# Performance work log

Hardware: AMD Instinct MI355X
Metric: run time of the kernel (lower is better)

Reference implementation:

```python
import jax, jax.numpy as jnp
import numpy as np

D, H_DIM, HEADS = 512, 2048, 8

def rmsnorm(x, w):
    eps = jnp.finfo(x.dtype).eps
    return x * jax.lax.rsqrt(jnp.mean(x * x, axis=-1, keepdims=True) + eps) * w

def setup_inputs() -> dict:
    key = jax.random.key(0)
    ks = jax.random.split(key, 16)
    B, N = 2, 2048
    s_d = 1.0 / np.sqrt(D)
    s_h = 1.0 / np.sqrt(H_DIM)
    inp = {
        "x": jax.random.normal(ks[0], (B, N, D), jnp.float32),
        "DA": jax.random.randint(ks[1], (B, 1, N, N), 0, 2, jnp.int32),
        "Wq": jax.random.normal(ks[2], (D, D), jnp.float32) * s_d,
        "bq": jnp.zeros((D,), jnp.float32),
        "Wk": jax.random.normal(ks[3], (D, D), jnp.float32) * s_d,
        "bk": jnp.zeros((D,), jnp.float32),
        "Wv": jax.random.normal(ks[4], (D, D), jnp.float32) * s_d,
        "bv": jnp.zeros((D,), jnp.float32),
        "W1": jax.random.normal(ks[5], (H_DIM, D), jnp.float32) * s_d,
        "b1": jnp.zeros((H_DIM,), jnp.float32),
        "W2": jax.random.normal(ks[6], (H_DIM, D), jnp.float32) * s_d,
        "b2": jnp.zeros((H_DIM,), jnp.float32),
        "W3": jax.random.normal(ks[7], (D, H_DIM), jnp.float32) * s_h,
        "b3": jnp.zeros((D,), jnp.float32),
        "g1": jnp.ones((D,), jnp.float32),
        "g2": jnp.ones((D,), jnp.float32),
    }
    return inp

def reference(x, DA, Wq, bq, Wk, bk, Wv, bv, W1, b1, W2, b2, W3, b3, g1, g2):
    B, N, _ = x.shape
    hd = D // HEADS  # head_dim = 64
    xn = rmsnorm(x, g1)
    # projections (torch Linear: y = x @ W.T + b), split heads -> [B,H,N,hd]
    def split(t):
        return t.reshape(B, N, HEADS, hd).transpose(0, 2, 1, 3)
    q = split(xn @ Wq.T + bq)
    k = split(xn @ Wk.T + bk)
    v = split(xn @ Wv.T + bv)
    scores = jnp.einsum("bhnd,bhmd->bhnm", q, k) / np.sqrt(hd)
    scores = jnp.where(DA == 0, jnp.asarray(-1e20, scores.dtype), scores)
    attn = jax.nn.softmax(scores, axis=-1)
    o = jnp.einsum("bhnm,bhmd->bhnd", attn, v)
    o = o.transpose(0, 2, 1, 3).reshape(B, N, D)
    h = x + o
    hn = rmsnorm(h, g2)
    x2 = hn @ W1.T + b1
    x3 = hn @ W2.T + b2
    out = h + (jax.nn.silu(x2) * x3) @ W3.T + b3
    return out
```

## Files before the change

kernel.cpp:

```cpp
#include <hip/hip_runtime.h>

typedef unsigned short u16;
typedef unsigned int   u32;
typedef unsigned long long u64;

using bf16x8 = __attribute__((ext_vector_type(8))) __bf16;
using f32x4  = __attribute__((ext_vector_type(4))) float;
using us8    = __attribute__((ext_vector_type(8))) u16;
using us4v   = __attribute__((ext_vector_type(4))) u16;

#define NB_TOK   4096
#define DD       512
#define HDIM     2048
#define SEQ      2048
#define EPS_F32  1.1920929e-7f
#define SM_SHIFT 16.0f

__device__ __forceinline__ u16 f32_to_bf16(float f) {
  u32 u = __float_as_uint(f);
  u += 0x7fffu + ((u >> 16) & 1u);
  return (u16)(u >> 16);
}
__device__ __forceinline__ float bf16_to_f32(u16 h) {
  return __uint_as_float(((u32)h) << 16);
}
__device__ __forceinline__ bf16x8 ld_frag(const u16* p) {
  return __builtin_bit_cast(bf16x8, *(const us8*)p);
}
__device__ __forceinline__ void gload_lds16(const void* g, void* l) {
  __builtin_amdgcn_global_load_lds(
      (__attribute__((address_space(1))) void*)(void*)g,
      (__attribute__((address_space(3))) void*)l, 16, 0, 0);
}

__global__ __launch_bounds__(256) void k_pre(
    const float* __restrict__ wq, const float* __restrict__ wk,
    const float* __restrict__ wv, const float* __restrict__ w1,
    const float* __restrict__ w2, const float* __restrict__ w3,
    const int* __restrict__ da, const float* __restrict__ x,
    const float* __restrict__ g1,
    u16* __restrict__ wqkv, u16* __restrict__ w1b,
    u16* __restrict__ w2b, u16* __restrict__ w3b,
    u64* __restrict__ maskT, u16* __restrict__ xn) {
  int bx = blockIdx.x;
  if (bx < 3840) {
    int e = (bx * 256 + threadIdx.x) * 4;
    const float* src; u16* dst; int off;
    if      (e <  262144) { src = wq; dst = wqkv;          off = e; }
    else if (e <  524288) { src = wk; dst = wqkv + 262144; off = e -  262144; }
    else if (e <  786432) { src = wv; dst = wqkv + 524288; off = e -  524288; }
    else if (e < 1835008) { src = w1; dst = w1b;           off = e -  786432; }
    else if (e < 2883584) { src = w2; dst = w2b;           off = e - 1835008; }
    else                  { src = w3; dst = w3b;           off = e - 2883584; }
    float4 v = *(const float4*)(src + off);
    us4v o;
    o[0] = f32_to_bf16(v.x); o[1] = f32_to_bf16(v.y);
    o[2] = f32_to_bf16(v.z); o[3] = f32_to_bf16(v.w);
    *(us4v*)(dst + off) = o;
  } else if (bx < 4864) {
    int lane = threadIdx.x & 63, wave = threadIdx.x >> 6;
    int row = (bx - 3840) * 4 + wave;
    int b = row >> 11, r = row & 2047;
    const int* src = da + (size_t)row * SEQ;
    #pragma unroll 4
    for (int w = 0; w < 32; ++w) {
      int d = src[w * 64 + lane];
      u64 bal = __ballot(d != 0);
      if (lane == 0) maskT[((size_t)(b * 32 + w)) * SEQ + r] = bal;
    }
  } else {
    int lane = threadIdx.x & 63, wave = threadIdx.x >> 6;
    int row = (bx - 4864) * 4 + wave;
    size_t base = (size_t)row * DD + lane * 8;
    float4 a = *(const float4*)(x + base);
    float4 b = *(const float4*)(x + base + 4);
    float ss = a.x*a.x + a.y*a.y + a.z*a.z + a.w*a.w
             + b.x*b.x + b.y*b.y + b.z*b.z + b.w*b.w;
    #pragma unroll
    for (int m = 1; m < 64; m <<= 1) ss += __shfl_xor(ss, m);
    float sc = rsqrtf(ss * (1.0f / DD) + EPS_F32);
    float4 ga = *(const float4*)(g1 + lane * 8);
    float4 gb = *(const float4*)(g1 + lane * 8 + 4);
    us8 o;
    o[0] = f32_to_bf16(a.x * sc * ga.x); o[1] = f32_to_bf16(a.y * sc * ga.y);
    o[2] = f32_to_bf16(a.z * sc * ga.z); o[3] = f32_to_bf16(a.w * sc * ga.w);
    o[4] = f32_to_bf16(b.x * sc * gb.x); o[5] = f32_to_bf16(b.y * sc * gb.y);
    o[6] = f32_to_bf16(b.z * sc * gb.z); o[7] = f32_to_bf16(b.w * sc * gb.w);
    *(us8*)(xn + base) = o;
  }
}

template <int NB>
__device__ __forceinline__ void gemm_tile(const u16* __restrict__ A,
                                          const u16* const* Bm, int K,
                                          int mblk, int nblk, int kbeg, int kend,
                                          u16* lA, u16* lB,
                                          f32x4 (*acc)[4][4]) {
  const int tid = threadIdx.x, lane = tid & 63, wave = tid >> 6;
  const int l15 = lane & 15, quad = lane >> 4;
  const int wm = (wave >> 1) * 64, wn = (wave & 1) * 64;
  for (int k0 = kbeg; k0 < kend; k0 += 32) {
    #pragma unroll
    for (int i = 0; i < 2; ++i) {
      int s = wave * 2 + i;
      int row = s * 16 + l15;
      gload_lds16(A + (size_t)(mblk + row) * K + k0 + quad * 8, lA + s * 512);
      #pragma unroll
      for (int bi = 0; bi < NB; ++bi)
        gload_lds16(Bm[bi] + (size_t)(nblk + row) * K + k0 + quad * 8,
                    lB + bi * 4096 + s * 512);
    }
    __syncthreads();
    bf16x8 af[4], bf[NB][4];
    #pragma unroll
    for (int mt = 0; mt < 4; ++mt)
      af[mt] = ld_frag(lA + ((wm >> 4) + mt) * 512 + lane * 8);
    #pragma unroll
    for (int bi = 0; bi < NB; ++bi)
      #pragma unroll
      for (int nt = 0; nt < 4; ++nt)
        bf[bi][nt] = ld_frag(lB + bi * 4096 + ((wn >> 4) + nt) * 512 + lane * 8);
    #pragma unroll
    for (int bi = 0; bi < NB; ++bi)
      #pragma unroll
      for (int mt = 0; mt < 4; ++mt)
        #pragma unroll
        for (int nt = 0; nt < 4; ++nt)
          acc[bi][mt][nt] = __builtin_amdgcn_mfma_f32_16x16x32_bf16(
              af[mt], bf[bi][nt], acc[bi][mt][nt], 0, 0, 0);
    __syncthreads();
  }
}

__global__ __launch_bounds__(256) void k_qkv(const u16* __restrict__ xn,
                                             const u16* __restrict__ wqkv,
                                             const float* __restrict__ bq,
                                             const float* __restrict__ bk,
                                             const float* __restrict__ bv,
                                             u16* __restrict__ qb,
                                             u16* __restrict__ kb,
                                             u16* __restrict__ vt) {
  __shared__ u16 lA[4096], lB[4096];
  int z = blockIdx.z;
  const u16* Bp = wqkv + z * (DD * DD);
  const float* bias = (z == 0) ? bq : ((z == 1) ? bk : bv);
  float scale = (z == 0) ? 0.125f : 1.0f;
  int mblk = blockIdx.y * 128, nblk = blockIdx.x * 128;
  f32x4 acc[1][4][4];
  #pragma unroll
  for (int mt = 0; mt < 4; ++mt)
    #pragma unroll
    for (int nt = 0; nt < 4; ++nt) acc[0][mt][nt] = (f32x4)0.0f;
  const u16* Bs[1] = {Bp};
  gemm_tile<1>(xn, Bs, DD, mblk, nblk, 0, DD, lA, lB, acc);
  int lane = threadIdx.x & 63, wave = threadIdx.x >> 6;
  int l15 = lane & 15, quad = lane >> 4;
  int wm = (wave >> 1) * 64, wn = (wave & 1) * 64;
  if (z < 2) {
    u16* out = z ? kb : qb;
    #pragma unroll
    for (int mt = 0; mt < 4; ++mt)
      #pragma unroll
      for (int nt = 0; nt < 4; ++nt) {
        int n = nblk + wn + nt * 16 + l15;
        float bn = bias[n];
        #pragma unroll
        for (int r = 0; r < 4; ++r) {
          int m = mblk + wm + mt * 16 + quad * 4 + r;
          out[(size_t)m * DD + n] = f32_to_bf16((acc[0][mt][nt][r] + bn) * scale);
        }
      }
  } else {
    #pragma unroll
    for (int mt = 0; mt < 4; ++mt)
      #pragma unroll
      for (int nt = 0; nt < 4; ++nt) {
        int n = nblk + wn + nt * 16 + l15;
        float bn = bias[n];
        int m = mblk + wm + mt * 16 + quad * 4;
        int b = m >> 11, tok = m & 2047;
        us4v o;
        #pragma unroll
        for (int r = 0; r < 4; ++r) o[r] = f32_to_bf16(acc[0][mt][nt][r] + bn);
        *(us4v*)(vt + ((size_t)(b * 8 + (n >> 6)) * 64 + (n & 63)) * SEQ + tok) = o;
      }
  }
}

__global__ __launch_bounds__(256) void k_attn(const u16* __restrict__ q,
                                              const u16* __restrict__ k,
                                              const u16* __restrict__ vT,
                                              const u64* __restrict__ maskT,
                                              float* __restrict__ Opart,
                                              float* __restrict__ lpart) {
  __shared__ u16 lQ[4096], lK[8192], lV[8192], lP[4 * 16 * 72];
  int tid = threadIdx.x, lane = tid & 63, wave = tid >> 6;
  int l15 = lane & 15, quad = lane >> 4;
  int bh = blockIdx.y, b = bh >> 3, h = bh & 7;
  int q0 = blockIdx.x * 64;
  int z = blockIdx.z;
  int kvbase = z * 1024;
  const u16* qg = q + (size_t)(b * SEQ + q0) * DD + h * 64;
  const u16* kg = k + (size_t)(b * SEQ + kvbase) * DD + h * 64;
  const u16* vg = vT + (size_t)bh * 64 * SEQ + kvbase;
  const u64* mg = maskT + ((size_t)(b * 32 + z * 16)) * SEQ + q0 + wave * 16 + l15;

  #pragma unroll
  for (int i = 0; i < 2; ++i) {
    int s = wave * 2 + i;
    int row = (s >> 1) * 16 + l15, c = (s & 1) * 4 + quad;
    gload_lds16(qg + (size_t)row * DD + c * 8, lQ + s * 512);
    gload_lds16(kg + (size_t)row * DD + c * 8, lK + s * 512);
    gload_lds16(vg + (size_t)row * SEQ + c * 8, lV + s * 512);
  }
  __syncthreads();
  bf16x8 qa[2];
  qa[0] = ld_frag(lQ + wave * 1024 + lane * 8);
  qa[1] = ld_frag(lQ + wave * 1024 + 512 + lane * 8);

  f32x4 oa[4];
  #pragma unroll
  for (int r = 0; r < 4; ++r) oa[r] = (f32x4)0.0f;
  float ls = 0.0f;

  u16* pw = lP + wave * 1152;

  for (int t = 0; t < 16; ++t) {
    const u16* lKc = lK + (t & 1) * 4096;
    const u16* lVc = lV + (t & 1) * 4096;

    u64 mw = mg[(size_t)t * SEQ];
    u64 mq = mw >> (quad * 4);

    if (t + 1 < 16) {
      int kv1 = (t + 1) * 64;
      u16* dK = lK + ((t + 1) & 1) * 4096;
      u16* dV = lV + ((t + 1) & 1) * 4096;
      #pragma unroll
      for (int i = 0; i < 2; ++i) {
        int s = wave * 2 + i;
        int row = (s >> 1) * 16 + l15, c = (s & 1) * 4 + quad;
        gload_lds16(kg + (size_t)(kv1 + row) * DD + c * 8, dK + s * 512);
        gload_lds16(vg + (size_t)row * SEQ + kv1 + c * 8, dV + s * 512);
      }
    }

    f32x4 sa[4];
    #pragma unroll
    for (int mt = 0; mt < 4; ++mt) sa[mt] = (f32x4)0.0f;
    #pragma unroll
    for (int ks = 0; ks < 2; ++ks) {
      bf16x8 ka[4];
      #pragma unroll
      for (int mt = 0; mt < 4; ++mt)
        ka[mt] = ld_frag(lKc + (mt * 2 + ks) * 512 + lane * 8);
      #pragma unroll
      for (int mt = 0; mt < 4; ++mt)
        sa[mt] = __builtin_amdgcn_mfma_f32_16x16x32_bf16(ka[mt], qa[ks], sa[mt], 0, 0, 0);
    }

    #pragma unroll
    for (int mt = 0; mt < 4; ++mt) {
      u32 nib = (u32)(mq >> (mt * 16)) & 0xFu;
      u32 pb[4];
      #pragma unroll
      for (int r = 0; r < 4; ++r) {
        float p = __expf(sa[mt][r] - SM_SHIFT);
        p = (nib >> r) & 1u ? p : 0.0f;
        u32 ub = __float_as_uint(p) & 0xffff0000u;
        ls += __uint_as_float(ub);
        pb[r] = ub;
      }
      u32 lo = __builtin_amdgcn_perm(pb[1], pb[0], 0x07060302u);
      u32 hi = __builtin_amdgcn_perm(pb[3], pb[2], 0x07060302u);
      u64 pk = ((u64)hi << 32) | lo;
      *(u64*)(pw + l15 * 72 + mt * 16 + quad * 4) = pk;
    }

    #pragma unroll
    for (int ks = 0; ks < 2; ++ks) {
      bf16x8 pa = ld_frag(pw + l15 * 72 + ks * 32 + quad * 8);
      bf16x8 vb[4];
      #pragma unroll
      for (int dt = 0; dt < 4; ++dt)
        vb[dt] = ld_frag(lVc + (dt * 2 + ks) * 512 + lane * 8);
      #pragma unroll
      for (int dt = 0; dt < 4; ++dt)
        oa[dt] = __builtin_amdgcn_mfma_f32_16x16x32_bf16(pa, vb[dt], oa[dt], 0, 0, 0);
    }

    __syncthreads();
  }

  ls += __shfl_xor(ls, 16);
  ls += __shfl_xor(ls, 32);
  if (quad == 0)
    lpart[((size_t)z * 16 + bh) * SEQ + q0 + wave * 16 + l15] = ls;

  float* Og = Opart + (size_t)z * NB_TOK * DD;
  #pragma unroll
  for (int r = 0; r < 4; ++r) {
    int m = q0 + wave * 16 + quad * 4 + r;
    float* dst = Og + (size_t)(b * SEQ + m) * DD + h * 64;
    #pragma unroll
    for (int dt = 0; dt < 4; ++dt)
      dst[dt * 16 + l15] = oa[dt][r];
  }
}

__global__ __launch_bounds__(256) void k_rms2(const float* __restrict__ x,
                                              const float* __restrict__ Opart,
                                              const float* __restrict__ lpart,
                                              const float* __restrict__ b3,
                                              const float* __restrict__ g2,
                                              float* __restrict__ outinit,
                                              u16* __restrict__ hn) {
  int lane = threadIdx.x & 63, wave = threadIdx.x >> 6;
  int row = blockIdx.x * 4 + wave;
  int b = row >> 11, tok = row & 2047, hh = lane >> 3;
  size_t base = (size_t)row * DD + lane * 8;
  float l0 = lpart[(size_t)(b * 8 + hh) * SEQ + tok];
  float l1 = lpart[(size_t)(16 + b * 8 + hh) * SEQ + tok];
  float lsum = l0 + l1;
  float inv = (lsum > 0.0f) ? (1.0f / lsum) : 0.0f;
  float4 a = *(const float4*)(x + base);
  float4 bb = *(const float4*)(x + base + 4);
  float4 o0a = *(const float4*)(Opart + base);
  float4 o0b = *(const float4*)(Opart + base + 4);
  float4 o1a = *(const float4*)(Opart + (size_t)NB_TOK * DD + base);
  float4 o1b = *(const float4*)(Opart + (size_t)NB_TOK * DD + base + 4);
  float hv[8];
  hv[0] = a.x  + (o0a.x + o1a.x) * inv;
  hv[1] = a.y  + (o0a.y + o1a.y) * inv;
  hv[2] = a.z  + (o0a.z + o1a.z) * inv;
  hv[3] = a.w  + (o0a.w + o1a.w) * inv;
  hv[4] = bb.x + (o0b.x + o1b.x) * inv;
  hv[5] = bb.y + (o0b.y + o1b.y) * inv;
  hv[6] = bb.z + (o0b.z + o1b.z) * inv;
  hv[7] = bb.w + (o0b.w + o1b.w) * inv;
  float ss = 0.0f;
  #pragma unroll
  for (int j = 0; j < 8; ++j) ss += hv[j] * hv[j];
  #pragma unroll
  for (int m = 1; m < 64; m <<= 1) ss += __shfl_xor(ss, m);
  float sc = rsqrtf(ss * (1.0f / DD) + EPS_F32);
  float4 c0 = *(const float4*)(b3 + lane * 8);
  float4 c1 = *(const float4*)(b3 + lane * 8 + 4);
  float4 w0 = {hv[0] + c0.x, hv[1] + c0.y, hv[2] + c0.z, hv[3] + c0.w};
  float4 w1 = {hv[4] + c1.x, hv[5] + c1.y, hv[6] + c1.z, hv[7] + c1.w};
  *(float4*)(outinit + base) = w0;
  *(float4*)(outinit + base + 4) = w1;
  float4 ga = *(const float4*)(g2 + lane * 8);
  float4 gb = *(const float4*)(g2 + lane * 8 + 4);
  us8 hb;
  hb[0] = f32_to_bf16(hv[0] * sc * ga.x); hb[1] = f32_to_bf16(hv[1] * sc * ga.y);
  hb[2] = f32_to_bf16(hv[2] * sc * ga.z); hb[3] = f32_to_bf16(hv[3] * sc * ga.w);
  hb[4] = f32_to_bf16(hv[4] * sc * gb.x); hb[5] = f32_to_bf16(hv[5] * sc * gb.y);
  hb[6] = f32_to_bf16(hv[6] * sc * gb.z); hb[7] = f32_to_bf16(hv[7] * sc * gb.w);
  *(us8*)(hn + base) = hb;
}

__global__ __launch_bounds__(256) void k_ffn12(const u16* __restrict__ hn,
                                               const u16* __restrict__ w1,
                                               const u16* __restrict__ w2,
                                               const float* __restrict__ b1,
                                               const float* __restrict__ b2,
                                               u16* __restrict__ g) {
  __shared__ u16 lA[4096], lB[8192];
  int mblk = blockIdx.y * 128, nblk = blockIdx.x * 128;
  f32x4 acc[2][4][4];
  #pragma unroll
  for (int bi = 0; bi < 2; ++bi)
    #pragma unroll
    for (int mt = 0; mt < 4; ++mt)
      #pragma unroll
      for (int nt = 0; nt < 4; ++nt) acc[bi][mt][nt] = (f32x4)0.0f;
  const u16* Bs[2] = {w1, w2};
  gemm_tile<2>(hn, Bs, DD, mblk, nblk, 0, DD, lA, lB, acc);
  int lane = threadIdx.x & 63, wave = threadIdx.x >> 6;
  int l15 = lane & 15, quad = lane >> 4;
  int wm = (wave >> 1) * 64, wn = (wave & 1) * 64;
  #pragma unroll
  for (int mt = 0; mt < 4; ++mt)
    #pragma unroll
    for (int nt = 0; nt < 4; ++nt) {
      int n = nblk + wn + nt * 16 + l15;
      float bb1 = b1[n], bb2 = b2[n];
      #pragma unroll
      for (int r = 0; r < 4; ++r) {
        int m = mblk + wm + mt * 16 + quad * 4 + r;
        float x2 = acc[0][mt][nt][r] + bb1;
        float x3 = acc[1][mt][nt][r] + bb2;
        float si = x2 / (1.0f + __expf(-x2));
        g[(size_t)m * HDIM + n] = f32_to_bf16(si * x3);
      }
    }
}

__global__ __launch_bounds__(256) void k_ffn3(const u16* __restrict__ g,
                                              const u16* __restrict__ w3,
                                              float* __restrict__ out) {
  __shared__ u16 lA[4096], lB[4096];
  int mblk = blockIdx.y * 128, nblk = blockIdx.x * 128, z = blockIdx.z;
  f32x4 acc[1][4][4];
  #pragma unroll
  for (int mt = 0; mt < 4; ++mt)
    #pragma unroll
    for (int nt = 0; nt < 4; ++nt) acc[0][mt][nt] = (f32x4)0.0f;
  const u16* Bs[1] = {w3};
  gemm_tile<1>(g, Bs, HDIM, mblk, nblk, z * 1024, z * 1024 + 1024, lA, lB, acc);
  int lane = threadIdx.x & 63, wave = threadIdx.x >> 6;
  int l15 = lane & 15, quad = lane >> 4;
  int wm = (wave >> 1) * 64, wn = (wave & 1) * 64;
  #pragma unroll
  for (int mt = 0; mt < 4; ++mt)
    #pragma unroll
    for (int nt = 0; nt < 4; ++nt) {
      int n = nblk + wn + nt * 16 + l15;
      #pragma unroll
      for (int r = 0; r < 4; ++r) {
        int m = mblk + wm + mt * 16 + quad * 4 + r;
        atomicAdd(out + (size_t)m * DD + n, acc[0][mt][nt][r]);
      }
    }
}

#define MB(x) ((size_t)(x) * 1048576)
#define WS_XN    MB(0)
#define WS_WQKV  MB(4)
#define WS_W1B   MB(6)
#define WS_W2B   MB(8)
#define WS_W3B   MB(10)
#define WS_MASK  MB(12)
#define WS_QB    MB(16)
#define WS_KB    MB(20)
#define WS_VT    MB(24)
#define WS_OP    MB(28)
#define WS_LP    MB(44)
#define WS_HN    MB(45)
#define WS_G     MB(49)

extern "C" void kernel_launch(void* const* d_in, const int* in_sizes, int n_in,
                              void* d_out, int out_size, void* d_ws, size_t ws_size,
                              hipStream_t stream) {
  (void)in_sizes; (void)n_in; (void)out_size; (void)ws_size;
  const float* x  = (const float*)d_in[0];
  const int*   DA = (const int*)d_in[1];
  const float* Wq = (const float*)d_in[2];
  const float* bq = (const float*)d_in[3];
  const float* Wk = (const float*)d_in[4];
  const float* bk = (const float*)d_in[5];
  const float* Wv = (const float*)d_in[6];
  const float* bv = (const float*)d_in[7];
  const float* W1 = (const float*)d_in[8];
  const float* b1 = (const float*)d_in[9];
  const float* W2 = (const float*)d_in[10];
  const float* b2 = (const float*)d_in[11];
  const float* W3 = (const float*)d_in[12];
  const float* b3 = (const float*)d_in[13];
  const float* g1 = (const float*)d_in[14];
  const float* g2 = (const float*)d_in[15];
  float* out = (float*)d_out;
  char* w = (char*)d_ws;

  u16* xn   = (u16*)(w + WS_XN);
  u16* wqkv = (u16*)(w + WS_WQKV);
  u16* w1b  = (u16*)(w + WS_W1B);
  u16* w2b  = (u16*)(w + WS_W2B);
  u16* w3b  = (u16*)(w + WS_W3B);
  u64* mskT = (u64*)(w + WS_MASK);
  u16* qb   = (u16*)(w + WS_QB);
  u16* kb   = (u16*)(w + WS_KB);
  u16* vt   = (u16*)(w + WS_VT);
  float* Op = (float*)(w + WS_OP);
  float* lp = (float*)(w + WS_LP);
  u16* hn   = (u16*)(w + WS_HN);
  u16* gb   = (u16*)(w + WS_G);

  k_pre<<<5888, 256, 0, stream>>>(Wq, Wk, Wv, W1, W2, W3, DA, x, g1,
                                  wqkv, w1b, w2b, w3b, mskT, xn);
  k_qkv<<<dim3(4, 32, 3), 256, 0, stream>>>(xn, wqkv, bq, bk, bv, qb, kb, vt);
  k_attn<<<dim3(32, 16, 2), 256, 0, stream>>>(qb, kb, vt, mskT, Op, lp);
  k_rms2<<<1024, 256, 0, stream>>>(x, Op, lp, b3, g2, out, hn);
  k_ffn12<<<dim3(16, 32), 256, 0, stream>>>(hn, w1b, w2b, b1, b2, gb);
  k_ffn3<<<dim3(4, 32, 2), 256, 0, stream>>>(gb, w3b, out);
}
```

Baseline: 299.0 us.

## Deepen GEMM K-step, double attention query tile, store partial outputs in bf16

Result: faster. 288.2 us (-3.6%).

```diff
diff --git a/kernel.cpp b/kernel.cpp
--- a/kernel.cpp
+++ b/kernel.cpp
@@ -91,43 +91,45 @@
 }
 
 template <int NB>
-__device__ __forceinline__ void gemm_tile(const u16* __restrict__ A,
-                                          const u16* const* Bm, int K,
-                                          int mblk, int nblk, int kbeg, int kend,
-                                          u16* lA, u16* lB,
-                                          f32x4 (*acc)[4][4]) {
+__device__ __forceinline__ void gemm64(const u16* __restrict__ A,
+                                       const u16* __restrict__ B0,
+                                       const u16* __restrict__ B1,
+                                       int K, int mblk, int nblk,
+                                       int kbeg, int kend,
+                                       u16* lA, u16* lB,
+                                       f32x4 (*acc)[4][4]) {
   const int tid = threadIdx.x, lane = tid & 63, wave = tid >> 6;
   const int l15 = lane & 15, quad = lane >> 4;
-  const int wm = (wave >> 1) * 64, wn = (wave & 1) * 64;
-  for (int k0 = kbeg; k0 < kend; k0 += 32) {
-    #pragma unroll
-    for (int i = 0; i < 2; ++i) {
-      int s = wave * 2 + i;
-      int row = s * 16 + l15;
-      gload_lds16(A + (size_t)(mblk + row) * K + k0 + quad * 8, lA + s * 512);
+  const int wmt = (wave >> 1) * 4, wnt = (wave & 1) * 4;
+  for (int k0 = kbeg; k0 < kend; k0 += 64) {
+    #pragma unroll
+    for (int i = 0; i < 4; ++i) {
+      int c = wave * 4 + i;
+      int mt = c >> 1, ks = c & 1;
+      size_t gofs = (size_t)(mt * 16 + l15) * K + k0 + ks * 32 + quad * 8;
+      gload_lds16(A + (size_t)mblk * K + gofs, lA + c * 512);
+      gload_lds16(B0 + (size_t)nblk * K + gofs, lB + c * 512);
+      if constexpr (NB == 2)
+        gload_lds16(B1 + (size_t)nblk * K + gofs, lB + 8192 + c * 512);
+    }
+    __syncthreads();
+    #pragma unroll
+    for (int ks = 0; ks < 2; ++ks) {
+      bf16x8 af[4];
+      #pragma unroll
+      for (int mt = 0; mt < 4; ++mt)
+        af[mt] = ld_frag(lA + (wmt + mt) * 1024 + ks * 512 + lane * 8);
       #pragma unroll
       for (int bi = 0; bi < NB; ++bi)
-        gload_lds16(Bm[bi] + (size_t)(nblk + row) * K + k0 + quad * 8,
-                    lB + bi * 4096 + s * 512);
-    }
-    __syncthreads();
-    bf16x8 af[4], bf[NB][4];
-    #pragma unroll
-    for (int mt = 0; mt < 4; ++mt)
-      af[mt] = ld_frag(lA + ((wm >> 4) + mt) * 512 + lane * 8);
-    #pragma unroll
-    for (int bi = 0; bi < NB; ++bi)
-      #pragma unroll
-      for (int nt = 0; nt < 4; ++nt)
-        bf[bi][nt] = ld_frag(lB + bi * 4096 + ((wn >> 4) + nt) * 512 + lane * 8);
-    #pragma unroll
-    for (int bi = 0; bi < NB; ++bi)
-      #pragma unroll
-      for (int mt = 0; mt < 4; ++mt)
         #pragma unroll
-        for (int nt = 0; nt < 4; ++nt)
-          acc[bi][mt][nt] = __builtin_amdgcn_mfma_f32_16x16x32_bf16(
-              af[mt], bf[bi][nt], acc[bi][mt][nt], 0, 0, 0);
+        for (int nt = 0; nt < 4; ++nt) {
+          bf16x8 b = ld_frag(lB + bi * 8192 + (wnt + nt) * 1024 + ks * 512 + lane * 8);
+          #pragma unroll
+          for (int mt = 0; mt < 4; ++mt)
+            acc[bi][mt][nt] = __builtin_amdgcn_mfma_f32_16x16x32_bf16(
+                af[mt], b, acc[bi][mt][nt], 0, 0, 0);
+        }
+    }
     __syncthreads();
   }
 }
@@ -140,19 +142,18 @@
                                              u16* __restrict__ qb,
                                              u16* __restrict__ kb,
                                              u16* __restrict__ vt) {
-  __shared__ u16 lA[4096], lB[4096];
+  __shared__ u16 lA[8192], lB[8192];
   int z = blockIdx.z;
   const u16* Bp = wqkv + z * (DD * DD);
   const float* bias = (z == 0) ? bq : ((z == 1) ? bk : bv);
   float scale = (z == 0) ? 0.125f : 1.0f;
-  int mblk = blockIdx.y * 128, nblk = blockIdx.x * 128;
+  int mblk = blockIdx.x * 128, nblk = blockIdx.y * 128;
   f32x4 acc[1][4][4];
   #pragma unroll
   for (int mt = 0; mt < 4; ++mt)
     #pragma unroll
     for (int nt = 0; nt < 4; ++nt) acc[0][mt][nt] = (f32x4)0.0f;
-  const u16* Bs[1] = {Bp};
-  gemm_tile<1>(xn, Bs, DD, mblk, nblk, 0, DD, lA, lB, acc);
+  gemm64<1>(xn, Bp, nullptr, DD, mblk, nblk, 0, DD, lA, lB, acc);
   int lane = threadIdx.x & 63, wave = threadIdx.x >> 6;
   int l15 = lane & 15, quad = lane >> 4;
   int wm = (wave >> 1) * 64, wn = (wave & 1) * 64;
@@ -191,46 +192,59 @@
                                               const u16* __restrict__ k,
                                               const u16* __restrict__ vT,
                                               const u64* __restrict__ maskT,
-                                              float* __restrict__ Opart,
+                                              u16* __restrict__ Opart,
                                               float* __restrict__ lpart) {
-  __shared__ u16 lQ[4096], lK[8192], lV[8192], lP[4 * 16 * 72];
+  __shared__ u16 lQ[8192], lK[8192], lV[8192], lP[4 * 32 * 72];
   int tid = threadIdx.x, lane = tid & 63, wave = tid >> 6;
   int l15 = lane & 15, quad = lane >> 4;
   int bh = blockIdx.y, b = bh >> 3, h = bh & 7;
-  int q0 = blockIdx.x * 64;
+  int q0 = blockIdx.x * 128;
   int z = blockIdx.z;
   int kvbase = z * 1024;
   const u16* qg = q + (size_t)(b * SEQ + q0) * DD + h * 64;
   const u16* kg = k + (size_t)(b * SEQ + kvbase) * DD + h * 64;
   const u16* vg = vT + (size_t)bh * 64 * SEQ + kvbase;
-  const u64* mg = maskT + ((size_t)(b * 32 + z * 16)) * SEQ + q0 + wave * 16 + l15;
-
+  const u64* mg = maskT + ((size_t)(b * 32 + z * 16)) * SEQ + q0 + wave * 32 + l15;
+
+  #pragma unroll
+  for (int i = 0; i < 4; ++i) {
+    int c = wave * 4 + i;
+    int nt = c >> 1, ks = c & 1;
+    gload_lds16(qg + (size_t)(nt * 16 + l15) * DD + ks * 32 + quad * 8, lQ + c * 512);
+  }
   #pragma unroll
   for (int i = 0; i < 2; ++i) {
-    int s = wave * 2 + i;
-    int row = (s >> 1) * 16 + l15, c = (s & 1) * 4 + quad;
-    gload_lds16(qg + (size_t)row * DD + c * 8, lQ + s * 512);
-    gload_lds16(kg + (size_t)row * DD + c * 8, lK + s * 512);
-    gload_lds16(vg + (size_t)row * SEQ + c * 8, lV + s * 512);
+    int c = wave * 2 + i;
+    int mt = c >> 1, ks = c & 1;
+    gload_lds16(kg + (size_t)(mt * 16 + l15) * DD + ks * 32 + quad * 8, lK + c * 512);
+    gload_lds16(vg + (size_t)(mt * 16 + l15) * SEQ + ks * 32 + quad * 8, lV + c * 512);
   }
   __syncthreads();
-  bf16x8 qa[2];
-  qa[0] = ld_frag(lQ + wave * 1024 + lane * 8);
-  qa[1] = ld_frag(lQ + wave * 1024 + 512 + lane * 8);
-
-  f32x4 oa[4];
-  #pragma unroll
-  for (int r = 0; r < 4; ++r) oa[r] = (f32x4)0.0f;
-  float ls = 0.0f;
-
-  u16* pw = lP + wave * 1152;
+
+  bf16x8 qa[2][2];
+  #pragma unroll
+  for (int nq = 0; nq < 2; ++nq)
+    #pragma unroll
+    for (int ks = 0; ks < 2; ++ks)
+      qa[nq][ks] = ld_frag(lQ + (wave * 2 + nq) * 1024 + ks * 512 + lane * 8);
+
+  f32x4 oa[2][4];
+  float ls[2] = {0.0f, 0.0f};
+  #pragma unroll
+  for (int mq = 0; mq < 2; ++mq)
+    #pragma unroll
+    for (int dt = 0; dt < 4; ++dt) oa[mq][dt] = (f32x4)0.0f;
+
+  u16* pw = lP + wave * 2304;
 
   for (int t = 0; t < 16; ++t) {
     const u16* lKc = lK + (t & 1) * 4096;
     const u16* lVc = lV + (t & 1) * 4096;
 
-    u64 mw = mg[(size_t)t * SEQ];
-    u64 mq = mw >> (quad * 4);
+    u64 mw[2];
+    #pragma unroll
+    for (int nq = 0; nq < 2; ++nq)
+      mw[nq] = mg[(size_t)t * SEQ + nq * 16] >> (quad * 4);
 
     if (t + 1 < 16) {
       int kv1 = (t + 1) * 64;
@@ -238,78 +252,95 @@
       u16* dV = lV + ((t + 1) & 1) * 4096;
       #pragma unroll
       for (int i = 0; i < 2; ++i) {
-        int s = wave * 2 + i;
-        int row = (s >> 1) * 16 + l15, c = (s & 1) * 4 + quad;
-        gload_lds16(kg + (size_t)(kv1 + row) * DD + c * 8, dK + s * 512);
-        gload_lds16(vg + (size_t)row * SEQ + kv1 + c * 8, dV + s * 512);
+        int c = wave * 2 + i;
+        int mt = c >> 1, ks = c & 1;
+        gload_lds16(kg + (size_t)(kv1 + mt * 16 + l15) * DD + ks * 32 + quad * 8, dK + c * 512);
+        gload_lds16(vg + (size_t)(mt * 16 + l15) * SEQ + kv1 + ks * 32 + quad * 8, dV + c * 512);
       }
     }
 
-    f32x4 sa[4];
-    #pragma unroll
-    for (int mt = 0; mt < 4; ++mt) sa[mt] = (f32x4)0.0f;
+    f32x4 sa[2][4];
+    #pragma unroll
+    for (int nq = 0; nq < 2; ++nq)
+      #pragma unroll
+      for (int mt = 0; mt < 4; ++mt) sa[nq][mt] = (f32x4)0.0f;
     #pragma unroll
     for (int ks = 0; ks < 2; ++ks) {
       bf16x8 ka[4];
       #pragma unroll
       for (int mt = 0; mt < 4; ++mt)
-        ka[mt] = ld_frag(lKc + (mt * 2 + ks) * 512 + lane * 8);
-      #pragma unroll
-      for (int mt = 0; mt < 4; ++mt)
-        sa[mt] = __builtin_amdgcn_mfma_f32_16x16x32_bf16(ka[mt], qa[ks], sa[mt], 0, 0, 0);
-    }
-
-    #pragma unroll
-    for (int mt = 0; mt < 4; ++mt) {
-      u32 nib = (u32)(mq >> (mt * 16)) & 0xFu;
-      u32 pb[4];
-      #pragma unroll
-      for (int r = 0; r < 4; ++r) {
-        float p = __expf(sa[mt][r] - SM_SHIFT);
-        p = (nib >> r) & 1u ? p : 0.0f;
-        u32 ub = __float_as_uint(p) & 0xffff0000u;
-        ls += __uint_as_float(ub);
-        pb[r] = ub;
+        ka[mt] = ld_frag(lKc + mt * 1024 + ks * 512 + lane * 8);
+      #pragma unroll
+      for (int nq = 0; nq < 2; ++nq)
+        #pragma unroll
+        for (int mt = 0; mt < 4; ++mt)
+          sa[nq][mt] = __builtin_amdgcn_mfma_f32_16x16x32_bf16(
+              ka[mt], qa[nq][ks], sa[nq][mt], 0, 0, 0);
+    }
+
+    #pragma unroll
+    for (int nq = 0; nq < 2; ++nq)
+      #pragma unroll
+      for (int mt = 0; mt < 4; ++mt) {
+        u32 nib = (u32)(mw[nq] >> (mt * 16)) & 0xFu;
+        u32 pb[4];
+        #pragma unroll
+        for (int r = 0; r < 4; ++r) {
+          float p = __expf(sa[nq][mt][r] - SM_SHIFT);
+          p = (nib >> r) & 1u ? p : 0.0f;
+          u32 ub = __float_as_uint(p) & 0xffff0000u;
+          ls[nq] += __uint_as_float(ub);
+          pb[r] = ub;
+        }
+        u32 lo = __builtin_amdgcn_perm(pb[1], pb[0], 0x07060302u);
+        u32 hi = __builtin_amdgcn_perm(pb[3], pb[2], 0x07060302u);
+        u64 pk = ((u64)hi << 32) | lo;
+        *(u64*)(pw + (nq * 16 + l15) * 72 + mt * 16 + quad * 4) = pk;
       }
-      u32 lo = __builtin_amdgcn_perm(pb[1], pb[0], 0x07060302u);
-      u32 hi = __builtin_amdgcn_perm(pb[3], pb[2], 0x07060302u);
-      u64 pk = ((u64)hi << 32) | lo;
-      *(u64*)(pw + l15 * 72 + mt * 16 + quad * 4) = pk;
-    }
 
     #pragma unroll
     for (int ks = 0; ks < 2; ++ks) {
-      bf16x8 pa = ld_frag(pw + l15 * 72 + ks * 32 + quad * 8);
-      bf16x8 vb[4];
+      bf16x8 pa[2], vb[4];
+      #pragma unroll
+      for (int mq = 0; mq < 2; ++mq)
+        pa[mq] = ld_frag(pw + (mq * 16 + l15) * 72 + ks * 32 + quad * 8);
       #pragma unroll
       for (int dt = 0; dt < 4; ++dt)
-        vb[dt] = ld_frag(lVc + (dt * 2 + ks) * 512 + lane * 8);
+        vb[dt] = ld_frag(lVc + dt * 1024 + ks * 512 + lane * 8);
+      #pragma unroll
+      for (int mq = 0; mq < 2; ++mq)
+        #pragma unroll
+        for (int dt = 0; dt < 4; ++dt)
+          oa[mq][dt] = __builtin_amdgcn_mfma_f32_16x16x32_bf16(
+              pa[mq], vb[dt], oa[mq][dt], 0, 0, 0);
+    }
+
+    __syncthreads();
+  }
+
+  #pragma unroll
+  for (int nq = 0; nq < 2; ++nq) {
+    ls[nq] += __shfl_xor(ls[nq], 16);
+    ls[nq] += __shfl_xor(ls[nq], 32);
+    if (quad == 0)
+      lpart[((size_t)z * 16 + bh) * SEQ + q0 + wave * 32 + nq * 16 + l15] = ls[nq];
+  }
+
+  u16* Og = Opart + (size_t)z * NB_TOK * DD;
+  #pragma unroll
+  for (int mq = 0; mq < 2; ++mq)
+    #pragma unroll
+    for (int r = 0; r < 4; ++r) {
+      int m = q0 + wave * 32 + mq * 16 + quad * 4 + r;
+      u16* dst = Og + (size_t)(b * SEQ + m) * DD + h * 64;
       #pragma unroll
       for (int dt = 0; dt < 4; ++dt)
-        oa[dt] = __builtin_amdgcn_mfma_f32_16x16x32_bf16(pa, vb[dt], oa[dt], 0, 0, 0);
-    }
-
-    __syncthreads();
-  }
-
-  ls += __shfl_xor(ls, 16);
-  ls += __shfl_xor(ls, 32);
-  if (quad == 0)
-    lpart[((size_t)z * 16 + bh) * SEQ + q0 + wave * 16 + l15] = ls;
-
-  float* Og = Opart + (size_t)z * NB_TOK * DD;
-  #pragma unroll
-  for (int r = 0; r < 4; ++r) {
-    int m = q0 + wave * 16 + quad * 4 + r;
-    float* dst = Og + (size_t)(b * SEQ + m) * DD + h * 64;
-    #pragma unroll
-    for (int dt = 0; dt < 4; ++dt)
-      dst[dt * 16 + l15] = oa[dt][r];
-  }
+        dst[dt * 16 + l15] = f32_to_bf16(oa[mq][dt][r]);
+    }
 }
 
 __global__ __launch_bounds__(256) void k_rms2(const float* __restrict__ x,
-                                              const float* __restrict__ Opart,
+                                              const u16* __restrict__ Opart,
                                               const float* __restrict__ lpart,
                                               const float* __restrict__ b3,
                                               const float* __restrict__ g2,
@@ -325,19 +356,17 @@
   float inv = (lsum > 0.0f) ? (1.0f / lsum) : 0.0f;
   float4 a = *(const float4*)(x + base);
   float4 bb = *(const float4*)(x + base + 4);
-  float4 o0a = *(const float4*)(Opart + base);
-  float4 o0b = *(const float4*)(Opart + base + 4);
-  float4 o1a = *(const float4*)(Opart + (size_t)NB_TOK * DD + base);
-  float4 o1b = *(const float4*)(Opart + (size_t)NB_TOK * DD + base + 4);
+  us8 o0 = *(const us8*)(Opart + base);
+  us8 o1 = *(const us8*)(Opart + (size_t)NB_TOK * DD + base);
   float hv[8];
-  hv[0] = a.x  + (o0a.x + o1a.x) * inv;
-  hv[1] = a.y  + (o0a.y + o1a.y) * inv;
-  hv[2] = a.z  + (o0a.z + o1a.z) * inv;
-  hv[3] = a.w  + (o0a.w + o1a.w) * inv;
-  hv[4] = bb.x + (o0b.x + o1b.x) * inv;
-  hv[5] = bb.y + (o0b.y + o1b.y) * inv;
-  hv[6] = bb.z + (o0b.z + o1b.z) * inv;
-  hv[7] = bb.w + (o0b.w + o1b.w) * inv;
+  hv[0] = a.x  + (bf16_to_f32(o0[0]) + bf16_to_f32(o1[0])) * inv;
+  hv[1] = a.y  + (bf16_to_f32(o0[1]) + bf16_to_f32(o1[1])) * inv;
+  hv[2] = a.z  + (bf16_to_f32(o0[2]) + bf16_to_f32(o1[2])) * inv;
+  hv[3] = a.w  + (bf16_to_f32(o0[3]) + bf16_to_f32(o1[3])) * inv;
+  hv[4] = bb.x + (bf16_to_f32(o0[4]) + bf16_to_f32(o1[4])) * inv;
+  hv[5] = bb.y + (bf16_to_f32(o0[5]) + bf16_to_f32(o1[5])) * inv;
+  hv[6] = bb.z + (bf16_to_f32(o0[6]) + bf16_to_f32(o1[6])) * inv;
+  hv[7] = bb.w + (bf16_to_f32(o0[7]) + bf16_to_f32(o1[7])) * inv;
   float ss = 0.0f;
   #pragma unroll
   for (int j = 0; j < 8; ++j) ss += hv[j] * hv[j];
@@ -366,8 +395,8 @@
                                                const float* __restrict__ b1,
                                                const float* __restrict__ b2,
                                                u16* __restrict__ g) {
-  __shared__ u16 lA[4096], lB[8192];
-  int mblk = blockIdx.y * 128, nblk = blockIdx.x * 128;
+  __shared__ u16 lA[8192], lB[16384];
+  int mblk = blockIdx.x * 128, nblk = blockIdx.y * 128;
   f32x4 acc[2][4][4];
   #pragma unroll
   for (int bi = 0; bi < 2; ++bi)
@@ -375,8 +404,7 @@
     for (int mt = 0; mt < 4; ++mt)
       #pragma unroll
       for (int nt = 0; nt < 4; ++nt) acc[bi][mt][nt] = (f32x4)0.0f;
-  const u16* Bs[2] = {w1, w2};
-  gemm_tile<2>(hn, Bs, DD, mblk, nblk, 0, DD, lA, lB, acc);
+  gemm64<2>(hn, w1, w2, DD, mblk, nblk, 0, DD, lA, lB, acc);
   int lane = threadIdx.x & 63, wave = threadIdx.x >> 6;
   int l15 = lane & 15, quad = lane >> 4;
   int wm = (wave >> 1) * 64, wn = (wave & 1) * 64;
@@ -400,15 +428,14 @@
 __global__ __launch_bounds__(256) void k_ffn3(const u16* __restrict__ g,
                                               const u16* __restrict__ w3,
                                               float* __restrict__ out) {
-  __shared__ u16 lA[4096], lB[4096];
-  int mblk = blockIdx.y * 128, nblk = blockIdx.x * 128, z = blockIdx.z;
+  __shared__ u16 lA[8192], lB[8192];
+  int mblk = blockIdx.x * 128, nblk = blockIdx.y * 128, z = blockIdx.z;
   f32x4 acc[1][4][4];
   #pragma unroll
   for (int mt = 0; mt < 4; ++mt)
     #pragma unroll
     for (int nt = 0; nt < 4; ++nt) acc[0][mt][nt] = (f32x4)0.0f;
-  const u16* Bs[1] = {w3};
-  gemm_tile<1>(g, Bs, HDIM, mblk, nblk, z * 1024, z * 1024 + 1024, lA, lB, acc);
+  gemm64<1>(g, w3, nullptr, HDIM, mblk, nblk, z * 512, z * 512 + 512, lA, lB, acc);
   int lane = threadIdx.x & 63, wave = threadIdx.x >> 6;
   int l15 = lane & 15, quad = lane >> 4;
   int wm = (wave >> 1) * 64, wn = (wave & 1) * 64;
@@ -472,16 +499,16 @@
   u16* qb   = (u16*)(w + WS_QB);
   u16* kb   = (u16*)(w + WS_KB);
   u16* vt   = (u16*)(w + WS_VT);
-  float* Op = (float*)(w + WS_OP);
+  u16* Op   = (u16*)(w + WS_OP);
   float* lp = (float*)(w + WS_LP);
   u16* hn   = (u16*)(w + WS_HN);
   u16* gb   = (u16*)(w + WS_G);
 
   k_pre<<<5888, 256, 0, stream>>>(Wq, Wk, Wv, W1, W2, W3, DA, x, g1,
                                   wqkv, w1b, w2b, w3b, mskT, xn);
-  k_qkv<<<dim3(4, 32, 3), 256, 0, stream>>>(xn, wqkv, bq, bk, bv, qb, kb, vt);
-  k_attn<<<dim3(32, 16, 2), 256, 0, stream>>>(qb, kb, vt, mskT, Op, lp);
+  k_qkv<<<dim3(32, 4, 3), 256, 0, stream>>>(xn, wqkv, bq, bk, bv, qb, kb, vt);
+  k_attn<<<dim3(16, 16, 2), 256, 0, stream>>>(qb, kb, vt, mskT, Op, lp);
   k_rms2<<<1024, 256, 0, stream>>>(x, Op, lp, b3, g2, out, hn);
-  k_ffn12<<<dim3(16, 32), 256, 0, stream>>>(hn, w1b, w2b, b1, b2, gb);
-  k_ffn3<<<dim3(4, 32, 2), 256, 0, stream>>>(gb, w3b, out);
-}
+  k_ffn12<<<dim3(32, 16), 256, 0, stream>>>(hn, w1b, w2b, b1, b2, gb);
+  k_ffn3<<<dim3(32, 4, 4), 256, 0, stream>>>(gb, w3b, out);
+}
```
